# Optimization experiments

Hardware: AMD Instinct MI355X
Metric: run time of the kernel (lower is better)

The kernel has to match this reference:

```python
import jax, jax.numpy as jnp
import numpy as np

EPS = 1e-8


def setup_inputs() -> dict:
    key = jax.random.key(0)
    ks = jax.random.split(key, 5)
    B, C, F, T = 2, 8, 1024, 256
    Ch, Fh = 4 * C, 4 * F  # expanded channels/features
    s_pw1 = 1.0 / np.sqrt(F)
    s_dw1 = 1.0 / np.sqrt(C)
    s_pw2 = 1.0 / np.sqrt(Fh)
    s_dw2 = 1.0 / np.sqrt(Ch)
    return {
        "x": jax.random.normal(ks[0], (B, C, F, T), jnp.float32),
        "ln_w": jnp.ones((C, F), jnp.float32),
        "ln_b": jnp.zeros((C, F), jnp.float32),
        "pw1": jax.random.uniform(ks[1], (C, Fh, F), jnp.float32, -s_pw1, s_pw1),
        "dw1": jax.random.uniform(ks[2], (Ch, C), jnp.float32, -s_dw1, s_dw1),
        "pw2": jax.random.uniform(ks[3], (Ch, F, Fh), jnp.float32, -s_pw2, s_pw2),
        "dw2": jax.random.uniform(ks[4], (C, Ch), jnp.float32, -s_dw2, s_dw2),
    }


def _mc_layernorm(x, w, b):
    # x: (B,C,F,T); normalize over feature axis (2), affine per (channel, feature)
    mu = jnp.mean(x, axis=2, keepdims=True)
    var = jnp.var(x, axis=2, keepdims=True)
    xn = (x - mu) * jax.lax.rsqrt(var + EPS)
    return xn * w[None, :, :, None] + b[None, :, :, None]


def reference(x, ln_w, ln_b, pw1, dw1, pw2, dw2):
    h = _mc_layernorm(x, ln_w, ln_b)
    # per-channel positionwise linear: (C, F_out, F_in)
    h = jnp.einsum('bcft,cgf->bcgt', h, pw1)
    # channel mixing (depthwise linear across channels): (C_out, C_in)
    h = jnp.einsum('bcft,dc->bdft', h, dw1)
    h = jnp.square(jax.nn.relu(h))  # squared ReLU
    h = jnp.einsum('bcft,cgf->bcgt', h, pw2)
    h = jnp.einsum('bcft,dc->bdft', h, dw2)
    return x + h
```

## Files before the change

kernel.cpp:

```cpp
#include <hip/hip_runtime.h>

#define B_DIM  2
#define C_DIM  8
#define F_DIM  1024
#define T_DIM  256
#define CH_DIM 32
#define FH_DIM 4096
#define BT_DIM 512

typedef __bf16 bf16x8 __attribute__((ext_vector_type(8)));
typedef __bf16 bf16x4 __attribute__((ext_vector_type(4)));
typedef float  f32x4  __attribute__((ext_vector_type(4)));

__device__ __forceinline__ void async16(const void* g, void* l) {
  __builtin_amdgcn_global_load_lds(
      (const __attribute__((address_space(1))) unsigned int*)g,
      (__attribute__((address_space(3))) unsigned int*)l, 16, 0, 0);
}

#define LGKM0_SCHED() do { \
    asm volatile("s_waitcnt lgkmcnt(0)" ::: "memory"); \
    __builtin_amdgcn_sched_barrier(0); } while (0)

__global__ void ln_kernel(const float* __restrict__ x,
                          const float* __restrict__ lnw,
                          const float* __restrict__ lnb,
                          __bf16* __restrict__ hn) {
  const int tb = blockIdx.x;
  const int c  = blockIdx.y;
  const int b  = blockIdx.z;
  const int tid = threadIdx.x;
  const int tx = tid & 15, ty = tid >> 4;
  const int t0 = tb * 16;

  const float* xp = x + (size_t)(b * C_DIM + c) * F_DIM * T_DIM;

  float s = 0.f, s2 = 0.f;
  for (int f = ty; f < F_DIM; f += 16) {
    float v = xp[f * T_DIM + t0 + tx];
    s += v; s2 += v * v;
  }
  __shared__ float ps[16][16], ps2[16][16];
  __shared__ float mean_s[16], rstd_s[16];
  ps[ty][tx] = s; ps2[ty][tx] = s2;
  __syncthreads();
  if (tid < 16) {
    float a = 0.f, a2 = 0.f;
    for (int j = 0; j < 16; ++j) { a += ps[j][tid]; a2 += ps2[j][tid]; }
    float mu  = a * (1.0f / F_DIM);
    float var = a2 * (1.0f / F_DIM) - mu * mu;
    mean_s[tid] = mu;
    rstd_s[tid] = rsqrtf(var + 1e-8f);
  }
  __syncthreads();

  __shared__ float tile[64][17];
  __bf16* hp = hn + ((size_t)c * BT_DIM + b * T_DIM + t0) * F_DIM;
  for (int ff = 0; ff < 16; ++ff) {
    const int f0 = ff * 64;
#pragma unroll
    for (int it = 0; it < 4; ++it) {
      int e  = it * 256 + tid;
      int fi = e >> 4, ti = e & 15;
      float v = xp[(f0 + fi) * T_DIM + t0 + ti];
      v = (v - mean_s[ti]) * rstd_s[ti];
      v = v * lnw[c * F_DIM + f0 + fi] + lnb[c * F_DIM + f0 + fi];
      tile[fi][ti] = v;
    }
    __syncthreads();
#pragma unroll
    for (int it = 0; it < 4; ++it) {
      int e  = it * 256 + tid;
      int fx = e & 63, tw = e >> 6;
      hp[(size_t)tw * F_DIM + f0 + fx] = (__bf16)tile[fx][tw];
    }
    __syncthreads();
  }
}

template<int MTBITS, bool CT>
__global__ __launch_bounds__(512, 2)
void gemm_bn512(const float* __restrict__ A, const __bf16* __restrict__ Bm,
                __bf16* __restrict__ Co, const int M, const int K) {
  const int bid = blockIdx.x;
  const int xcd = bid & 7, idx = bid >> 3;
  const int batch = xcd * (32 >> MTBITS) + (idx >> MTBITS);
  const int mt    = idx & ((1 << MTBITS) - 1);

  const int tid = threadIdx.x, lane = tid & 63, wid = tid >> 6;

  const float*  Ab = A  + (size_t)batch * M * K + (size_t)(mt * 128) * K;
  const __bf16* Bb = Bm + (size_t)batch * BT_DIM * K;

  extern __shared__ __align__(16) char smem[];
  __bf16* const AS = (__bf16*)smem;
  __bf16* const BS = (__bf16*)(smem + 16384);

  const int a_r = tid >> 2, a_q = tid & 3;
  const int a_swz = a_q ^ ((a_r >> 1) & 3);
  const float* const aBase = Ab + (size_t)a_r * K + a_q * 8;

  const int b_r0 = wid * 64 + (lane >> 2);
  const int b_s  = (lane & 3) ^ ((lane >> 3) & 3);

  const int wm = wid >> 2, wn = wid & 3;
  const int lr = lane & 15, khi = lane >> 4;
  const int rsw = (lr >> 1) & 3;

  f32x4 acc[4][8] = {};
  float4 sa[2];
  const int NT = K >> 5;

  auto issueA = [&](int tt) {
    sa[0] = *(const float4*)(aBase + (size_t)tt * 32);
    sa[1] = *(const float4*)(aBase + (size_t)tt * 32 + 4);
  };
  auto writeA = [&](int buf) {
    bf16x8 v;
    v[0]=(__bf16)sa[0].x; v[1]=(__bf16)sa[0].y; v[2]=(__bf16)sa[0].z; v[3]=(__bf16)sa[0].w;
    v[4]=(__bf16)sa[1].x; v[5]=(__bf16)sa[1].y; v[6]=(__bf16)sa[1].z; v[7]=(__bf16)sa[1].w;
    *(bf16x8*)(AS + buf * 4096 + a_r * 32 + a_swz * 8) = v;
  };
  auto issueB = [&](int buf, int tt) {
#pragma unroll
    for (int j = 0; j < 4; ++j) {
      const int r = b_r0 + j * 16;
      async16(Bb + (size_t)r * K + (size_t)tt * 32 + b_s * 8,
              BS + buf * 16384 + (wid * 64 + j * 16) * 32);
    }
  };
  auto compute = [&](int buf) {
    const __bf16* As = AS + buf * 4096;
    const __bf16* Bs = BS + buf * 16384;
    const int so = (khi ^ rsw) << 3;
    bf16x8 af[4];
#pragma unroll
    for (int mi = 0; mi < 4; ++mi)
      af[mi] = *(const bf16x8*)(As + (wm * 64 + mi * 16 + lr) * 32 + so);
#pragma unroll
    for (int h = 0; h < 2; ++h) {
      bf16x8 bq[4];
#pragma unroll
      for (int nj = 0; nj < 4; ++nj)
        bq[nj] = *(const bf16x8*)(Bs + (wn * 128 + (h * 4 + nj) * 16 + lr) * 32 + so);
      __builtin_amdgcn_s_setprio(1);
#pragma unroll
      for (int mi = 0; mi < 4; ++mi)
#pragma unroll
        for (int nj = 0; nj < 4; ++nj)
          acc[mi][h * 4 + nj] =
              __builtin_amdgcn_mfma_f32_16x16x32_bf16(af[mi], bq[nj], acc[mi][h * 4 + nj], 0, 0, 0);
      __builtin_amdgcn_s_setprio(0);
    }
  };

  issueA(0);
  issueB(0, 0);
  writeA(0);
  asm volatile("s_waitcnt vmcnt(0) lgkmcnt(0)" ::: "memory");
  __builtin_amdgcn_s_barrier();
  __builtin_amdgcn_sched_barrier(0);

  int buf = 0;
  for (int t = 0; t < NT; ++t) {
    const int tn = (t + 1 < NT) ? t + 1 : t;
    issueA(tn);
    issueB(buf ^ 1, tn);
    compute(buf);
    writeA(buf ^ 1);
    asm volatile("s_waitcnt vmcnt(0) lgkmcnt(0)" ::: "memory");
    __builtin_amdgcn_s_barrier();
    __builtin_amdgcn_sched_barrier(0);
    buf ^= 1;
  }

  const int colc = lane & 15;
  const int rowb = (lane >> 4) * 4;
  if (CT) {
    __bf16* T = (__bf16*)smem + wid * 1152;
    const int mbase = mt * 128 + wm * 64;
#pragma unroll
    for (int ni = 0; ni < 8; ++ni) {
#pragma unroll
      for (int mi = 0; mi < 4; ++mi)
#pragma unroll
        for (int r = 0; r < 4; ++r)
          T[colc * 72 + mi * 16 + rowb + r] = (__bf16)acc[mi][ni][r];
      __bf16* outp = Co + (size_t)batch * BT_DIM * M
                        + (size_t)(wn * 128 + ni * 16) * M + mbase + lane;
#pragma unroll
      for (int r16 = 0; r16 < 16; ++r16)
        outp[(size_t)r16 * M] = T[r16 * 72 + lane];
    }
  } else {
#pragma unroll
    for (int mi = 0; mi < 4; ++mi) {
#pragma unroll
      for (int ni = 0; ni < 8; ++ni) {
        const int m = mt * 128 + wm * 64 + mi * 16 + rowb;
        const int n = wn * 128 + ni * 16 + colc;
#pragma unroll
        for (int r = 0; r < 4; ++r)
          Co[((size_t)batch * M + m + r) * BT_DIM + n] = (__bf16)acc[mi][ni][r];
      }
    }
  }
}

__global__ __launch_bounds__(512, 2)
void gemm_pw2_8p(const float* __restrict__ A, const __bf16* __restrict__ Bm,
                 __bf16* __restrict__ Co) {
  const int M = F_DIM, K = FH_DIM;
  const int NT = K >> 6;
  const int bid = blockIdx.x;
  const int xcd = bid & 7, idx = bid >> 3;
  const int batch = xcd * 4 + (idx >> 3);
  const int tile  = idx & 7;
  const int mt = tile >> 1, nt = tile & 1;

  const int tid = threadIdx.x, lane = tid & 63, wid = tid >> 6;

  const float*  Ab = A  + (size_t)batch * M * K + (size_t)(mt * 256) * K;
  const __bf16* Bb = Bm + (size_t)batch * BT_DIM * K + (size_t)(nt * 256) * K;

  extern __shared__ __align__(16) char smem[];
  __bf16* const AS = (__bf16*)smem;
  __bf16* const BS = (__bf16*)(smem + 65536);

  const int wm = wid >> 2, wn = wid & 3;
  const int lr = lane & 15, khi = lane >> 4;
  const int lsw = lr & 7;

  const int b_row = lane >> 3;
  const int b_src = (lane & 7) ^ b_row;

  f32x4 acc[8][4] = {};
  float4 sa[8];
  bf16x8 af[4];

  auto issueB1 = [&](int sbuf, int tt, int j) {
    const int chunk = j * 8 + wid;
    async16(Bb + (size_t)(chunk * 8 + b_row) * K + (size_t)tt * 64 + b_src * 8,
            BS + sbuf * 16384 + chunk * 512);
  };
  auto issueA2 = [&](int tt, int i0) {
#pragma unroll
    for (int i = i0; i < i0 + 2; ++i) {
      const int c = i * 512 + tid;
      sa[i] = *(const float4*)(Ab + (size_t)(c >> 4) * K + (size_t)tt * 64 + (c & 15) * 4);
    }
  };
  auto writeA2 = [&](int abuf, int i0) {
#pragma unroll
    for (int i = i0; i < i0 + 2; ++i) {
      const int c = i * 512 + tid;
      const int r = c >> 4;
      const int s = ((c & 15) >> 1) ^ (r & 7);
      bf16x4 v;
      v[0]=(__bf16)sa[i].x; v[1]=(__bf16)sa[i].y; v[2]=(__bf16)sa[i].z; v[3]=(__bf16)sa[i].w;
      *(bf16x4*)(AS + abuf * 16384 + r * 64 + s * 8 + (c & 1) * 4) = v;
    }
  };
  auto readA = [&](int abuf, int mq, int ks) {
#pragma unroll
    for (int j = 0; j < 4; ++j) {
      const int row = wm * 128 + (mq * 4 + j) * 16 + lr;
      af[j] = *(const bf16x8*)(AS + abuf * 16384 + row * 64 + (((ks << 2) | khi) ^ lsw) * 8);
    }
  };
  auto readB2 = [&](bf16x8* bq, int rbuf, int np, int ks) {
#pragma unroll
    for (int j = 0; j < 2; ++j) {
      const int row = wn * 64 + (np * 2 + j) * 16 + lr;
      bq[j] = *(const bf16x8*)(BS + rbuf * 16384 + row * 64 + (((ks << 2) | khi) ^ lsw) * 8);
    }
  };
  auto mfma8 = [&](const bf16x8* bq, int mq, int np) {
    __builtin_amdgcn_s_setprio(1);
#pragma unroll
    for (int j = 0; j < 4; ++j)
#pragma unroll
      for (int n = 0; n < 2; ++n)
        acc[mq * 4 + j][np * 2 + n] =
            __builtin_amdgcn_mfma_f32_16x16x32_bf16(af[j], bq[n], acc[mq * 4 + j][np * 2 + n], 0, 0, 0);
    __builtin_amdgcn_s_setprio(0);
  };

  issueA2(0, 0); issueA2(0, 2); issueA2(0, 4); issueA2(0, 6);
  issueB1(0, 0, 0); issueB1(0, 0, 1); issueB1(0, 0, 2); issueB1(0, 0, 3);
  issueB1(1, 1, 0); issueB1(1, 1, 1); issueB1(1, 1, 2); issueB1(1, 1, 3);
  writeA2(0, 0); writeA2(0, 2); writeA2(0, 4); writeA2(0, 6);
  issueA2(1, 0); issueA2(1, 2); issueA2(1, 4); issueA2(1, 6);
  asm volatile("s_waitcnt vmcnt(12)" ::: "memory");
  LGKM0_SCHED();
  __builtin_amdgcn_s_barrier();

  int cur = 0;
  for (int t = 0; t < NT; ++t) {
    const int rd = t % 3, st = (t + 2) % 3;
    const int tN = (t + 2 < NT) ? t + 2 : NT - 1;
    bf16x8 bq[2];
    issueB1(st, tN, 0);
    readA(cur, 0, 0); readB2(bq, rd, 0, 0);
    __builtin_amdgcn_s_barrier(); LGKM0_SCHED();
    mfma8(bq, 0, 0); __builtin_amdgcn_s_barrier();
    issueB1(st, tN, 1);
    readB2(bq, rd, 1, 0);
    __builtin_amdgcn_s_barrier(); LGKM0_SCHED();
    mfma8(bq, 0, 1); __builtin_amdgcn_s_barrier();
    issueB1(st, tN, 2);
    readA(cur, 1, 0); readB2(bq, rd, 0, 0);
    __builtin_amdgcn_s_barrier(); LGKM0_SCHED();
    mfma8(bq, 1, 0); __builtin_amdgcn_s_barrier();
    issueB1(st, tN, 3);
    readB2(bq, rd, 1, 0);
    __builtin_amdgcn_s_barrier(); LGKM0_SCHED();
    mfma8(bq, 1, 1); __builtin_amdgcn_s_barrier();
    writeA2(cur ^ 1, 0); issueA2(tN, 0);
    readA(cur, 0, 1); readB2(bq, rd, 0, 1);
    __builtin_amdgcn_s_barrier(); LGKM0_SCHED();
    mfma8(bq, 0, 0); __builtin_amdgcn_s_barrier();
    writeA2(cur ^ 1, 2); issueA2(tN, 2);
    readB2(bq, rd, 1, 1);
    __builtin_amdgcn_s_barrier(); LGKM0_SCHED();
    mfma8(bq, 0, 1); __builtin_amdgcn_s_barrier();
    writeA2(cur ^ 1, 4); issueA2(tN, 4);
    readA(cur, 1, 1); readB2(bq, rd, 0, 1);
    __builtin_amdgcn_s_barrier(); LGKM0_SCHED();
    mfma8(bq, 1, 0); __builtin_amdgcn_s_barrier();
    writeA2(cur ^ 1, 6); issueA2(tN, 6);
    readB2(bq, rd, 1, 1);
    __builtin_amdgcn_s_barrier(); LGKM0_SCHED();
    mfma8(bq, 1, 1);
    __builtin_amdgcn_s_barrier();
    cur ^= 1;
  }

  const int colc = lane & 15;
  const int rowb = (lane >> 4) * 4;
#pragma unroll
  for (int mi = 0; mi < 8; ++mi) {
#pragma unroll
    for (int ni = 0; ni < 4; ++ni) {
      const int m = mt * 256 + wm * 128 + mi * 16 + rowb;
      const int n = nt * 256 + wn * 64 + ni * 16 + colc;
#pragma unroll
      for (int r = 0; r < 4; ++r)
        Co[((size_t)batch * M + m + r) * BT_DIM + n] = (__bf16)acc[mi][ni][r];
    }
  }
}

__global__ void mix1_kernel(const __bf16* __restrict__ Y1,
                            const float* __restrict__ dw1,
                            __bf16* __restrict__ h2) {
  const int gidx = blockIdx.x * 256 + threadIdx.x;
  const int g8 = gidx & 511, bt = gidx >> 9;
  const int g0 = g8 * 8;

  float y[C_DIM][8];
#pragma unroll
  for (int c = 0; c < C_DIM; ++c) {
    bf16x8 v = *(const bf16x8*)(Y1 + ((size_t)c * BT_DIM + bt) * FH_DIM + g0);
#pragma unroll
    for (int j = 0; j < 8; ++j) y[c][j] = (float)v[j];
  }
  for (int d = 0; d < CH_DIM; ++d) {
    float s[8] = {0.f,0.f,0.f,0.f,0.f,0.f,0.f,0.f};
#pragma unroll
    for (int c = 0; c < C_DIM; ++c) {
      const float wv = dw1[d * C_DIM + c];
#pragma unroll
      for (int j = 0; j < 8; ++j) s[j] += wv * y[c][j];
    }
    bf16x8 o;
#pragma unroll
    for (int j = 0; j < 8; ++j) {
      float r = s[j] > 0.f ? s[j] : 0.f;
      o[j] = (__bf16)(r * r);
    }
    *(bf16x8*)(h2 + ((size_t)d * BT_DIM + bt) * FH_DIM + g0) = o;
  }
}

__global__ void mix2_kernel(const float* __restrict__ x,
                            const __bf16* __restrict__ Y2,
                            const float* __restrict__ dw2,
                            float* __restrict__ out) {
  const int gidx = blockIdx.x * 256 + threadIdx.x;
  const int t4 = gidx & 63;
  const int f  = (gidx >> 6) & 1023;
  const int b  = gidx >> 16;
  const int t0 = t4 * 4;

  float4 r[C_DIM];
#pragma unroll
  for (int dd = 0; dd < C_DIM; ++dd)
    r[dd] = *(const float4*)(x + ((size_t)(b * C_DIM + dd) * F_DIM + f) * T_DIM + t0);

  for (int d = 0; d < CH_DIM; ++d) {
    bf16x4 v = *(const bf16x4*)(Y2 + ((size_t)d * F_DIM + f) * BT_DIM + b * T_DIM + t0);
    const float v0 = (float)v[0], v1 = (float)v[1], v2 = (float)v[2], v3 = (float)v[3];
#pragma unroll
    for (int dd = 0; dd < C_DIM; ++dd) {
      const float w = dw2[dd * CH_DIM + d];
      r[dd].x += w * v0; r[dd].y += w * v1; r[dd].z += w * v2; r[dd].w += w * v3;
    }
  }
#pragma unroll
  for (int dd = 0; dd < C_DIM; ++dd)
    *(float4*)(out + ((size_t)(b * C_DIM + dd) * F_DIM + f) * T_DIM + t0) = r[dd];
}

extern "C" void kernel_launch(void* const* d_in, const int* in_sizes, int n_in,
                              void* d_out, int out_size, void* d_ws, size_t ws_size,
                              hipStream_t stream) {
  const float* x   = (const float*)d_in[0];
  const float* lnw = (const float*)d_in[1];
  const float* lnb = (const float*)d_in[2];
  const float* pw1 = (const float*)d_in[3];
  const float* dw1 = (const float*)d_in[4];
  const float* pw2 = (const float*)d_in[5];
  const float* dw2 = (const float*)d_in[6];
  float* out = (float*)d_out;

  char* ws = (char*)d_ws;
  __bf16* hn = (__bf16*)(ws);
  __bf16* Y1 = (__bf16*)(ws + (8ULL << 20));
  __bf16* h2 = (__bf16*)(ws + (40ULL << 20));
  __bf16* Y2 = (__bf16*)(ws);

  (void)hipFuncSetAttribute((const void*)gemm_bn512<5, true>,
                            hipFuncAttributeMaxDynamicSharedMemorySize, 81920);
  (void)hipFuncSetAttribute((const void*)gemm_pw2_8p,
                            hipFuncAttributeMaxDynamicSharedMemorySize, 163840);

  ln_kernel<<<dim3(T_DIM / 16, C_DIM, B_DIM), 256, 0, stream>>>(x, lnw, lnb, hn);
  gemm_bn512<5, true><<<256, 512, 81920, stream>>>(pw1, hn, Y1, FH_DIM, F_DIM);
  mix1_kernel<<<(BT_DIM * (FH_DIM / 8)) / 256, 256, 0, stream>>>(Y1, dw1, h2);
  gemm_pw2_8p<<<256, 512, 163840, stream>>>(pw2, h2, Y2);
  mix2_kernel<<<512, 256, 0, stream>>>(x, Y2, dw2, out);
}
```

Measured before the change: 333.3 us.

## Reuse the 8-phase 256x256 GEMM kernel for the pw1 projection

The separate 128x512-tile pw1 GEMM is dropped. The 8-phase pipelined 256x256-tile kernel already used for pw2 is generalised with a tiles-per-batch template parameter and runtime M/K, then used for both GEMMs. A transposed-store epilogue (staged through LDS) is added to the shared kernel for the pw1 output layout. The aim is better operand reuse and latency hiding on the larger-K pipeline. In exchange, the pw1 GEMM now needs 160KB of LDS, which limits it to one block per CU.

```diff
diff --git a/kernel.cpp b/kernel.cpp
--- a/kernel.cpp
+++ b/kernel.cpp
@@ -78,144 +78,15 @@
   }
 }
 
-template<int MTBITS, bool CT>
+template<int TPB_BITS, bool CT>
 __global__ __launch_bounds__(512, 2)
-void gemm_bn512(const float* __restrict__ A, const __bf16* __restrict__ Bm,
-                __bf16* __restrict__ Co, const int M, const int K) {
-  const int bid = blockIdx.x;
-  const int xcd = bid & 7, idx = bid >> 3;
-  const int batch = xcd * (32 >> MTBITS) + (idx >> MTBITS);
-  const int mt    = idx & ((1 << MTBITS) - 1);
-
-  const int tid = threadIdx.x, lane = tid & 63, wid = tid >> 6;
-
-  const float*  Ab = A  + (size_t)batch * M * K + (size_t)(mt * 128) * K;
-  const __bf16* Bb = Bm + (size_t)batch * BT_DIM * K;
-
-  extern __shared__ __align__(16) char smem[];
-  __bf16* const AS = (__bf16*)smem;
-  __bf16* const BS = (__bf16*)(smem + 16384);
-
-  const int a_r = tid >> 2, a_q = tid & 3;
-  const int a_swz = a_q ^ ((a_r >> 1) & 3);
-  const float* const aBase = Ab + (size_t)a_r * K + a_q * 8;
-
-  const int b_r0 = wid * 64 + (lane >> 2);
-  const int b_s  = (lane & 3) ^ ((lane >> 3) & 3);
-
-  const int wm = wid >> 2, wn = wid & 3;
-  const int lr = lane & 15, khi = lane >> 4;
-  const int rsw = (lr >> 1) & 3;
-
-  f32x4 acc[4][8] = {};
-  float4 sa[2];
-  const int NT = K >> 5;
-
-  auto issueA = [&](int tt) {
-    sa[0] = *(const float4*)(aBase + (size_t)tt * 32);
-    sa[1] = *(const float4*)(aBase + (size_t)tt * 32 + 4);
-  };
-  auto writeA = [&](int buf) {
-    bf16x8 v;
-    v[0]=(__bf16)sa[0].x; v[1]=(__bf16)sa[0].y; v[2]=(__bf16)sa[0].z; v[3]=(__bf16)sa[0].w;
-    v[4]=(__bf16)sa[1].x; v[5]=(__bf16)sa[1].y; v[6]=(__bf16)sa[1].z; v[7]=(__bf16)sa[1].w;
-    *(bf16x8*)(AS + buf * 4096 + a_r * 32 + a_swz * 8) = v;
-  };
-  auto issueB = [&](int buf, int tt) {
-#pragma unroll
-    for (int j = 0; j < 4; ++j) {
-      const int r = b_r0 + j * 16;
-      async16(Bb + (size_t)r * K + (size_t)tt * 32 + b_s * 8,
-              BS + buf * 16384 + (wid * 64 + j * 16) * 32);
-    }
-  };
-  auto compute = [&](int buf) {
-    const __bf16* As = AS + buf * 4096;
-    const __bf16* Bs = BS + buf * 16384;
-    const int so = (khi ^ rsw) << 3;
-    bf16x8 af[4];
-#pragma unroll
-    for (int mi = 0; mi < 4; ++mi)
-      af[mi] = *(const bf16x8*)(As + (wm * 64 + mi * 16 + lr) * 32 + so);
-#pragma unroll
-    for (int h = 0; h < 2; ++h) {
-      bf16x8 bq[4];
-#pragma unroll
-      for (int nj = 0; nj < 4; ++nj)
-        bq[nj] = *(const bf16x8*)(Bs + (wn * 128 + (h * 4 + nj) * 16 + lr) * 32 + so);
-      __builtin_amdgcn_s_setprio(1);
-#pragma unroll
-      for (int mi = 0; mi < 4; ++mi)
-#pragma unroll
-        for (int nj = 0; nj < 4; ++nj)
-          acc[mi][h * 4 + nj] =
-              __builtin_amdgcn_mfma_f32_16x16x32_bf16(af[mi], bq[nj], acc[mi][h * 4 + nj], 0, 0, 0);
-      __builtin_amdgcn_s_setprio(0);
-    }
-  };
-
-  issueA(0);
-  issueB(0, 0);
-  writeA(0);
-  asm volatile("s_waitcnt vmcnt(0) lgkmcnt(0)" ::: "memory");
-  __builtin_amdgcn_s_barrier();
-  __builtin_amdgcn_sched_barrier(0);
-
-  int buf = 0;
-  for (int t = 0; t < NT; ++t) {
-    const int tn = (t + 1 < NT) ? t + 1 : t;
-    issueA(tn);
-    issueB(buf ^ 1, tn);
-    compute(buf);
-    writeA(buf ^ 1);
-    asm volatile("s_waitcnt vmcnt(0) lgkmcnt(0)" ::: "memory");
-    __builtin_amdgcn_s_barrier();
-    __builtin_amdgcn_sched_barrier(0);
-    buf ^= 1;
-  }
-
-  const int colc = lane & 15;
-  const int rowb = (lane >> 4) * 4;
-  if (CT) {
-    __bf16* T = (__bf16*)smem + wid * 1152;
-    const int mbase = mt * 128 + wm * 64;
-#pragma unroll
-    for (int ni = 0; ni < 8; ++ni) {
-#pragma unroll
-      for (int mi = 0; mi < 4; ++mi)
-#pragma unroll
-        for (int r = 0; r < 4; ++r)
-          T[colc * 72 + mi * 16 + rowb + r] = (__bf16)acc[mi][ni][r];
-      __bf16* outp = Co + (size_t)batch * BT_DIM * M
-                        + (size_t)(wn * 128 + ni * 16) * M + mbase + lane;
-#pragma unroll
-      for (int r16 = 0; r16 < 16; ++r16)
-        outp[(size_t)r16 * M] = T[r16 * 72 + lane];
-    }
-  } else {
-#pragma unroll
-    for (int mi = 0; mi < 4; ++mi) {
-#pragma unroll
-      for (int ni = 0; ni < 8; ++ni) {
-        const int m = mt * 128 + wm * 64 + mi * 16 + rowb;
-        const int n = wn * 128 + ni * 16 + colc;
-#pragma unroll
-        for (int r = 0; r < 4; ++r)
-          Co[((size_t)batch * M + m + r) * BT_DIM + n] = (__bf16)acc[mi][ni][r];
-      }
-    }
-  }
-}
-
-__global__ __launch_bounds__(512, 2)
-void gemm_pw2_8p(const float* __restrict__ A, const __bf16* __restrict__ Bm,
-                 __bf16* __restrict__ Co) {
-  const int M = F_DIM, K = FH_DIM;
+void gemm_8p(const float* __restrict__ A, const __bf16* __restrict__ Bm,
+             __bf16* __restrict__ Co, const int M, const int K) {
   const int NT = K >> 6;
   const int bid = blockIdx.x;
   const int xcd = bid & 7, idx = bid >> 3;
-  const int batch = xcd * 4 + (idx >> 3);
-  const int tile  = idx & 7;
+  const int batch = xcd * (32 >> TPB_BITS) + (idx >> TPB_BITS);
+  const int tile  = idx & ((1 << TPB_BITS) - 1);
   const int mt = tile >> 1, nt = tile & 1;
 
   const int tid = threadIdx.x, lane = tid & 63, wid = tid >> 6;
@@ -338,15 +209,36 @@
 
   const int colc = lane & 15;
   const int rowb = (lane >> 4) * 4;
-#pragma unroll
-  for (int mi = 0; mi < 8; ++mi) {
-#pragma unroll
-    for (int ni = 0; ni < 4; ++ni) {
-      const int m = mt * 256 + wm * 128 + mi * 16 + rowb;
-      const int n = nt * 256 + wn * 64 + ni * 16 + colc;
-#pragma unroll
-      for (int r = 0; r < 4; ++r)
-        Co[((size_t)batch * M + m + r) * BT_DIM + n] = (__bf16)acc[mi][ni][r];
+  if (CT) {
+    __bf16* T = (__bf16*)smem + wid * 1152;
+#pragma unroll
+    for (int h = 0; h < 2; ++h) {
+      const int mbase = mt * 256 + wm * 128 + h * 64;
+#pragma unroll
+      for (int ni = 0; ni < 4; ++ni) {
+#pragma unroll
+        for (int mi = 0; mi < 4; ++mi)
+#pragma unroll
+          for (int r = 0; r < 4; ++r)
+            T[colc * 72 + mi * 16 + rowb + r] = (__bf16)acc[h * 4 + mi][ni][r];
+        __bf16* outp = Co + (size_t)batch * BT_DIM * M
+                          + (size_t)(nt * 256 + wn * 64 + ni * 16) * M + mbase + lane;
+#pragma unroll
+        for (int r16 = 0; r16 < 16; ++r16)
+          outp[(size_t)r16 * M] = T[r16 * 72 + lane];
+      }
+    }
+  } else {
+#pragma unroll
+    for (int mi = 0; mi < 8; ++mi) {
+#pragma unroll
+      for (int ni = 0; ni < 4; ++ni) {
+        const int m = mt * 256 + wm * 128 + mi * 16 + rowb;
+        const int n = nt * 256 + wn * 64 + ni * 16 + colc;
+#pragma unroll
+        for (int r = 0; r < 4; ++r)
+          Co[((size_t)batch * M + m + r) * BT_DIM + n] = (__bf16)acc[mi][ni][r];
+      }
     }
   }
 }
@@ -430,14 +322,14 @@
   __bf16* h2 = (__bf16*)(ws + (40ULL << 20));
   __bf16* Y2 = (__bf16*)(ws);
 
-  (void)hipFuncSetAttribute((const void*)gemm_bn512<5, true>,
-                            hipFuncAttributeMaxDynamicSharedMemorySize, 81920);
-  (void)hipFuncSetAttribute((const void*)gemm_pw2_8p,
+  (void)hipFuncSetAttribute((const void*)gemm_8p<5, true>,
                             hipFuncAttributeMaxDynamicSharedMemorySize, 163840);
+  (void)hipFuncSetAttribute((const void*)gemm_8p<3, false>,
+                            hipFuncAttributeMaxDynamicSharedMemorySize, 163840);
 
   ln_kernel<<<dim3(T_DIM / 16, C_DIM, B_DIM), 256, 0, stream>>>(x, lnw, lnb, hn);
-  gemm_bn512<5, true><<<256, 512, 81920, stream>>>(pw1, hn, Y1, FH_DIM, F_DIM);
+  gemm_8p<5, true><<<256, 512, 163840, stream>>>(pw1, hn, Y1, FH_DIM, F_DIM);
   mix1_kernel<<<(BT_DIM * (FH_DIM / 8)) / 256, 256, 0, stream>>>(Y1, dw1, h2);
-  gemm_pw2_8p<<<256, 512, 163840, stream>>>(pw2, h2, Y2);
+  gemm_8p<3, false><<<256, 512, 163840, stream>>>(pw2, h2, Y2, F_DIM, FH_DIM);
   mix2_kernel<<<512, 256, 0, stream>>>(x, Y2, dw2, out);
 }
```

Result: faster. 316.7 us (-5.0%).
